# Performance work log

Hardware: AMD Instinct MI355X
Metric: run time of the kernel (lower is better)

The kernel has to match this reference:

```python
import jax, jax.numpy as jnp
import numpy as np

B, C, H, W = 4, 256, 128, 128
D = 256            # attention hidden_dim (== C, so no output_proj)
HID = 1024         # mlp hidden = int(C * 4.0)
EPS = 1e-5


def setup_inputs() -> dict:
    key = jax.random.key(0)
    ks = jax.random.split(key, 16)
    s = 0.02
    return {
        "x": jax.random.normal(ks[0], (B, C, H, W), jnp.float32),
        "wq": jax.random.normal(ks[1], (C, D), jnp.float32) * s,
        "bq": jnp.zeros((D,), jnp.float32),
        "wk": jax.random.normal(ks[2], (C, D), jnp.float32) * s,
        "bk": jnp.zeros((D,), jnp.float32),
        "wv": jax.random.normal(ks[3], (C, D), jnp.float32) * s,
        "bv": jnp.zeros((D,), jnp.float32),
        "ln1_g": jnp.ones((C,), jnp.float32),
        "ln1_b": jnp.zeros((C,), jnp.float32),
        "ln2_g": jnp.ones((C,), jnp.float32),
        "ln2_b": jnp.zeros((C,), jnp.float32),
        "fc1_w": jax.random.normal(ks[4], (C, HID), jnp.float32) * s,
        "fc1_b": jnp.zeros((HID,), jnp.float32),
        "fc2_w": jax.random.normal(ks[5], (HID, C), jnp.float32) * s,
        "fc2_b": jnp.zeros((C,), jnp.float32),
    }


def _layernorm(x, g, b):
    m = jnp.mean(x, axis=-1, keepdims=True)
    v = jnp.mean(jnp.square(x - m), axis=-1, keepdims=True)
    return (x - m) * jax.lax.rsqrt(v + EPS) * g + b


def _neighborhoods(t):
    # t: [B,H,W,D] -> [B,H,W,9,D] 3x3 neighborhoods, zero-padded at borders
    tp = jnp.pad(t, ((0, 0), (1, 1), (1, 1), (0, 0)))
    h, w = t.shape[1], t.shape[2]
    return jnp.stack(
        [tp[:, dy:dy + h, dx:dx + w, :] for dy in range(3) for dx in range(3)],
        axis=3,
    )


def _valid_mask(h, w):
    # [H,W,9] bool: which of the 9 neighbors are inside the grid
    ys = jnp.arange(h)[:, None] * jnp.ones((1, w), jnp.int32)
    xs = jnp.arange(w)[None, :] * jnp.ones((h, 1), jnp.int32)
    top, bot = ys > 0, ys < h - 1
    lef, rig = xs > 0, xs < w - 1
    ones = jnp.ones((h, w), bool)
    return jnp.stack(
        [top & lef, top, top & rig, lef, ones, rig, bot & lef, bot, bot & rig],
        axis=-1,
    )


def reference(x, wq, bq, wk, bk, wv, bv, ln1_g, ln1_b, ln2_g, ln2_b,
              fc1_w, fc1_b, fc2_w, fc2_b):
    b_, c_, h_, w_ = x.shape
    xc = jnp.transpose(x, (0, 2, 3, 1))                    # [B,H,W,C]
    n1 = _layernorm(xc, ln1_g, ln1_b)
    q = n1 @ wq + bq                                       # [B,H,W,D]
    k = n1 @ wk + bk
    v = n1 @ wv + bv
    kn = _neighborhoods(k)                                  # [B,H,W,9,D]
    vn = _neighborhoods(v)
    scores = jnp.einsum('bhwd,bhwnd->bhwn', q, kn) / jnp.sqrt(jnp.float32(q.shape[-1]))
    mask = _valid_mask(h_, w_)                               # [H,W,9]
    scores = jnp.where(mask, scores, jnp.float32(-1e9))
    weights = jax.nn.softmax(scores, axis=-1)
    attn = jnp.einsum('bhwn,bhwnd->bhwd', weights, vn)       # [B,H,W,D]
    x1 = xc + attn                                           # residual 1
    n2 = _layernorm(x1, ln2_g, ln2_b)
    mlp = jax.nn.gelu(n2 @ fc1_w + fc1_b, approximate=False) @ fc2_w + fc2_b
    out = x1 + mlp
    return jnp.transpose(out, (0, 3, 1, 2))                  # [B,C,H,W]
```

## Files before the change

### kernel.cpp

```cpp
#include <hip/hip_runtime.h>
#include <hip/hip_bf16.h>
#include <math.h>

#define NPIX  65536
#define CCH   256
#define HWSZ  16384
#define WIDTH 128
#define HID   1024

typedef unsigned short u16;
typedef __bf16 bf16x8 __attribute__((ext_vector_type(8)));
typedef float  floatx4 __attribute__((ext_vector_type(4)));

__device__ __forceinline__ float bf2f(u16 u) {
  union { unsigned int i; float f; } c; c.i = ((unsigned int)u) << 16; return c.f;
}
__device__ __forceinline__ float bflo(unsigned int u) {
  union { unsigned int i; float f; } c; c.i = u << 16; return c.f;
}
__device__ __forceinline__ float bfhi(unsigned int u) {
  union { unsigned int i; float f; } c; c.i = u & 0xffff0000u; return c.f;
}
__device__ __forceinline__ u16 f2bf(float f) {
  union { float f; unsigned int i; } c; c.f = f;
  unsigned int x = c.i;
  x += 0x7fffu + ((x >> 16) & 1u);
  return (u16)(x >> 16);
}

__device__ __forceinline__ void async16(const void* g, void* l) {
  __builtin_amdgcn_global_load_lds(
      (const __attribute__((address_space(1))) void*)g,
      (__attribute__((address_space(3))) void*)l, 16, 0, 0);
}

__global__ __launch_bounds__(256) void wtrans_kernel(
    const float* __restrict__ src, u16* __restrict__ dst, int R, int C) {
  __shared__ float tile[32][33];
  const int tx = threadIdx.x & 31, ty = threadIdx.x >> 5;
  const int r0 = blockIdx.y * 32, c0 = blockIdx.x * 32;
#pragma unroll
  for (int i = 0; i < 32; i += 8)
    tile[ty + i][tx] = src[(size_t)(r0 + ty + i) * C + c0 + tx];
  __syncthreads();
#pragma unroll
  for (int i = 0; i < 32; i += 8)
    dst[(size_t)(c0 + ty + i) * R + r0 + tx] = f2bf(tile[tx][ty + i]);
}

__global__ __launch_bounds__(256) void ln1_kernel(
    const float* __restrict__ x, const float* __restrict__ g,
    const float* __restrict__ bb, u16* __restrict__ n1) {
  __shared__ float sx[32][257];
  __shared__ float sred[16][32];
  __shared__ float sm[32], sr[32];
  const int tx = threadIdx.x;
  const int p0 = blockIdx.x * 32;
  {
    const int pix = tx & 31, cpart = tx >> 5;
    const int p = p0 + pix;
    const int b = p >> 14, hw = p & (HWSZ - 1);
    const float* xb = x + ((size_t)b * CCH) * HWSZ + hw;
    float s = 0.f, s2 = 0.f;
#pragma unroll 4
    for (int i = 0; i < 32; i++) {
      const int c = cpart * 32 + i;
      const float v = xb[(size_t)c * HWSZ];
      sx[pix][c] = v;
      s += v; s2 += v * v;
    }
    sred[cpart][pix] = s; sred[8 + cpart][pix] = s2;
  }
  __syncthreads();
  if (tx < 32) {
    float s = 0.f, s2 = 0.f;
#pragma unroll
    for (int j = 0; j < 8; j++) { s += sred[j][tx]; s2 += sred[8 + j][tx]; }
    const float m = s * (1.0f / 256.0f);
    const float var = s2 * (1.0f / 256.0f) - m * m;
    sm[tx] = m; sr[tx] = rsqrtf(var + 1e-5f);
  }
  __syncthreads();
  const float gc = g[tx], bc = bb[tx];
#pragma unroll 4
  for (int i = 0; i < 32; i++) {
    const float v = (sx[i][tx] - sm[i]) * sr[i] * gc + bc;
    n1[(size_t)(p0 + i) * CCH + tx] = f2bf(v);
  }
}

__global__ __launch_bounds__(256) void res_ln2_kernel(
    const float* __restrict__ x, const u16* __restrict__ attn,
    const float* __restrict__ g, const float* __restrict__ bb,
    float* __restrict__ x1, u16* __restrict__ n2) {
  __shared__ float sx[32][257];
  __shared__ float sred[16][32];
  __shared__ float sm[32], sr[32];
  const int tx = threadIdx.x;
  const int p0 = blockIdx.x * 32;
  {
    const int pix = tx & 31, cpart = tx >> 5;
    const int p = p0 + pix;
    const int b = p >> 14, hw = p & (HWSZ - 1);
    const float* xb = x + ((size_t)b * CCH) * HWSZ + hw;
#pragma unroll 4
    for (int i = 0; i < 32; i++) {
      const int c = cpart * 32 + i;
      sx[pix][c] = xb[(size_t)c * HWSZ];
    }
  }
  __syncthreads();
#pragma unroll 4
  for (int i = 0; i < 32; i++) {
    const float v = sx[i][tx] + bf2f(attn[(size_t)(p0 + i) * CCH + tx]);
    sx[i][tx] = v;
    x1[(size_t)(p0 + i) * CCH + tx] = v;
  }
  __syncthreads();
  {
    const int pix = tx & 31, cpart = tx >> 5;
    float s = 0.f, s2 = 0.f;
#pragma unroll 4
    for (int i = 0; i < 32; i++) {
      const float v = sx[pix][cpart * 32 + i];
      s += v; s2 += v * v;
    }
    sred[cpart][pix] = s; sred[8 + cpart][pix] = s2;
  }
  __syncthreads();
  if (tx < 32) {
    float s = 0.f, s2 = 0.f;
#pragma unroll
    for (int j = 0; j < 8; j++) { s += sred[j][tx]; s2 += sred[8 + j][tx]; }
    const float m = s * (1.0f / 256.0f);
    const float var = s2 * (1.0f / 256.0f) - m * m;
    sm[tx] = m; sr[tx] = rsqrtf(var + 1e-5f);
  }
  __syncthreads();
  const float gc = g[tx], bc = bb[tx];
#pragma unroll 4
  for (int i = 0; i < 32; i++) {
    const float v = (sx[i][tx] - sm[i]) * sr[i] * gc + bc;
    n2[(size_t)(p0 + i) * CCH + tx] = f2bf(v);
  }
}

__global__ __launch_bounds__(256) void attn_kernel(
    const u16* __restrict__ q, const u16* __restrict__ k,
    const u16* __restrict__ v, u16* __restrict__ attn) {
  const int tid = threadIdx.x;
  const int wave = tid >> 6, lane = tid & 63;
  const int p = blockIdx.x * 4 + wave;
  const int hw = p & (HWSZ - 1);
  const int hh = hw >> 7, ww = hw & (WIDTH - 1);
  const size_t co = (size_t)p * CCH + lane * 4;
  const uint2 qr = *(const uint2*)(q + co);
  const float qf0 = bflo(qr.x), qf1 = bfhi(qr.x);
  const float qf2 = bflo(qr.y), qf3 = bfhi(qr.y);
  float sc[9];
#pragma unroll
  for (int n = 0; n < 9; n++) {
    const int dy = n / 3 - 1, dx = n % 3 - 1;
    const int y = hh + dy, x2 = ww + dx;
    float s = -1e30f;
    if (y >= 0 && y < 128 && x2 >= 0 && x2 < 128) {
      const uint2 kr = *(const uint2*)(k + co + dy * (WIDTH * CCH) + dx * CCH);
      float d = qf0 * bflo(kr.x) + qf1 * bfhi(kr.x)
              + qf2 * bflo(kr.y) + qf3 * bfhi(kr.y);
#pragma unroll
      for (int o = 32; o >= 1; o >>= 1) d += __shfl_xor(d, o, 64);
      s = d * 0.0625f;
    }
    sc[n] = s;
  }
  float mx = sc[0];
#pragma unroll
  for (int n = 1; n < 9; n++) mx = fmaxf(mx, sc[n]);
  float wgt[9], wsum = 0.f;
#pragma unroll
  for (int n = 0; n < 9; n++) { wgt[n] = __expf(sc[n] - mx); wsum += wgt[n]; }
  const float inv = 1.0f / wsum;
  float a0 = 0.f, a1 = 0.f, a2 = 0.f, a3 = 0.f;
#pragma unroll
  for (int n = 0; n < 9; n++) {
    const int dy = n / 3 - 1, dx = n % 3 - 1;
    const int y = hh + dy, x2 = ww + dx;
    if (y >= 0 && y < 128 && x2 >= 0 && x2 < 128) {
      const uint2 vr = *(const uint2*)(v + co + dy * (WIDTH * CCH) + dx * CCH);
      const float wn = wgt[n] * inv;
      a0 += wn * bflo(vr.x); a1 += wn * bfhi(vr.x);
      a2 += wn * bflo(vr.y); a3 += wn * bfhi(vr.y);
    }
  }
  uint2 o;
  o.x = ((unsigned int)f2bf(a1) << 16) | (unsigned int)f2bf(a0);
  o.y = ((unsigned int)f2bf(a3) << 16) | (unsigned int)f2bf(a2);
  *(uint2*)(attn + co) = o;
}

template <int EPI>
__global__ __launch_bounds__(256, 2) void gemm_kernel(
    const u16* __restrict__ A, const u16* __restrict__ BT,
    const float* __restrict__ bias, const float* __restrict__ x1,
    u16* __restrict__ outb, float* __restrict__ outf, int K, int Nn) {
  __shared__ u16 sA[4096];
  __shared__ u16 sB[4096];
  const int tid = threadIdx.x;
  const int wave = tid >> 6;
  const int lane = tid & 63;
  const int quad = lane >> 4;
  const int l16 = lane & 15;
  const int m0 = blockIdx.x * 128;
  const int n0 = blockIdx.y * 128;
  const int wr = (wave >> 1) * 64;
  const int wc = (wave & 1) * 64;

  floatx4 acc[4][4];
#pragma unroll
  for (int i = 0; i < 4; i++)
#pragma unroll
    for (int j = 0; j < 4; j++) acc[i][j] = (floatx4){0.f, 0.f, 0.f, 0.f};

  const int ci0 = tid, ci1 = tid + 256;
  const u16* aP0 = A + (size_t)(m0 + (ci0 >> 2)) * K + (ci0 & 3) * 8;
  const u16* aP1 = A + (size_t)(m0 + (ci1 >> 2)) * K + (ci1 & 3) * 8;
  const u16* bP0 = BT + (size_t)(n0 + (ci0 >> 2)) * K + (ci0 & 3) * 8;
  const u16* bP1 = BT + (size_t)(n0 + (ci1 >> 2)) * K + (ci1 & 3) * 8;
  u16* sA0 = &sA[(wave * 64) * 8];
  u16* sA1 = &sA[(256 + wave * 64) * 8];
  u16* sB0 = &sB[(wave * 64) * 8];
  u16* sB1 = &sB[(256 + wave * 64) * 8];

  for (int k0 = 0; k0 < K; k0 += 32) {
    async16(aP0 + k0, sA0);
    async16(aP1 + k0, sA1);
    async16(bP0 + k0, sB0);
    async16(bP1 + k0, sB1);
    __syncthreads();
    bf16x8 af[4], bfv[4];
#pragma unroll
    for (int mi = 0; mi < 4; mi++)
      af[mi] = *(const bf16x8*)&sA[(wr + mi * 16 + l16) * 32 + quad * 8];
#pragma unroll
    for (int ni = 0; ni < 4; ni++)
      bfv[ni] = *(const bf16x8*)&sB[(wc + ni * 16 + l16) * 32 + quad * 8];
#pragma unroll
    for (int mi = 0; mi < 4; mi++)
#pragma unroll
      for (int ni = 0; ni < 4; ni++)
        acc[mi][ni] = __builtin_amdgcn_mfma_f32_16x16x32_bf16(
            af[mi], bfv[ni], acc[mi][ni], 0, 0, 0);
    __syncthreads();
  }

#pragma unroll
  for (int mi = 0; mi < 4; mi++) {
#pragma unroll
    for (int ni = 0; ni < 4; ni++) {
      const int col = n0 + wc + ni * 16 + l16;
      const float bs = bias[col];
#pragma unroll
      for (int r = 0; r < 4; r++) {
        const int row = m0 + wr + mi * 16 + quad * 4 + r;
        float val = acc[mi][ni][r] + bs;
        if (EPI == 0) {
          outb[(size_t)row * Nn + col] = f2bf(val);
        } else if (EPI == 1) {
          val = 0.5f * val * (1.0f + erff(val * 0.70710678118654752f));
          outb[(size_t)row * Nn + col] = f2bf(val);
        } else {
          val += x1[(size_t)row * CCH + col];
          const int b = row >> 14, hw = row & (HWSZ - 1);
          outf[((size_t)(b * CCH + col)) * HWSZ + hw] = val;
        }
      }
    }
  }
}

extern "C" void kernel_launch(void* const* d_in, const int* in_sizes, int n_in,
                              void* d_out, int out_size, void* d_ws, size_t ws_size,
                              hipStream_t stream) {
  const float* x    = (const float*)d_in[0];
  const float* wq   = (const float*)d_in[1];
  const float* bq   = (const float*)d_in[2];
  const float* wk   = (const float*)d_in[3];
  const float* bk   = (const float*)d_in[4];
  const float* wv   = (const float*)d_in[5];
  const float* bv   = (const float*)d_in[6];
  const float* ln1g = (const float*)d_in[7];
  const float* ln1b = (const float*)d_in[8];
  const float* ln2g = (const float*)d_in[9];
  const float* ln2b = (const float*)d_in[10];
  const float* fc1w = (const float*)d_in[11];
  const float* fc1b = (const float*)d_in[12];
  const float* fc2w = (const float*)d_in[13];
  const float* fc2b = (const float*)d_in[14];
  float* out = (float*)d_out;

  char* ws = (char*)d_ws;
  const size_t MB = (size_t)1 << 20;
  float* x1  = (float*)(ws);
  u16* hbuf  = (u16*)(ws + 64 * MB);
  u16* kbuf  = (u16*)(ws + 64 * MB);
  u16* vbuf  = (u16*)(ws + 96 * MB);
  u16* n1    = (u16*)(ws + 128 * MB);
  u16* attnb = n1;
  u16* qbuf  = (u16*)(ws + 192 * MB);
  u16* n2    = qbuf;
  u16* wqT   = (u16*)(ws + 224 * MB);
  u16* wkT   = wqT + 256 * 256;
  u16* wvT   = wkT + 256 * 256;
  u16* f1T   = wvT + 256 * 256;
  u16* f2T   = f1T + 1024 * 256;

  dim3 blk(256);
  wtrans_kernel<<<dim3(8, 8), blk, 0, stream>>>(wq, wqT, 256, 256);
  wtrans_kernel<<<dim3(8, 8), blk, 0, stream>>>(wk, wkT, 256, 256);
  wtrans_kernel<<<dim3(8, 8), blk, 0, stream>>>(wv, wvT, 256, 256);
  wtrans_kernel<<<dim3(32, 8), blk, 0, stream>>>(fc1w, f1T, 256, 1024);
  wtrans_kernel<<<dim3(8, 32), blk, 0, stream>>>(fc2w, f2T, 1024, 256);

  ln1_kernel<<<NPIX / 32, blk, 0, stream>>>(x, ln1g, ln1b, n1);

  gemm_kernel<0><<<dim3(512, 2), blk, 0, stream>>>(n1, wqT, bq, nullptr, qbuf, nullptr, 256, 256);
  gemm_kernel<0><<<dim3(512, 2), blk, 0, stream>>>(n1, wkT, bk, nullptr, kbuf, nullptr, 256, 256);
  gemm_kernel<0><<<dim3(512, 2), blk, 0, stream>>>(n1, wvT, bv, nullptr, vbuf, nullptr, 256, 256);

  attn_kernel<<<NPIX / 4, blk, 0, stream>>>(qbuf, kbuf, vbuf, attnb);

  res_ln2_kernel<<<NPIX / 32, blk, 0, stream>>>(x, attnb, ln2g, ln2b, x1, n2);

  gemm_kernel<1><<<dim3(512, 8), blk, 0, stream>>>(n2, f1T, fc1b, nullptr, hbuf, nullptr, 256, HID);
  gemm_kernel<2><<<dim3(512, 2), blk, 0, stream>>>(hbuf, f2T, fc2b, x1, nullptr, out, HID, 256);
}
```

Before: 489.4 us.

## Fuse QKV GEMMs, keep A tile in registers, use tanh GELU

Concatenates the Q/K/V weights and biases so a single GEMM writes an interleaved [pix,768] QKV buffer, and adapts the attention kernel to read from it. Replaces the old LDS-tiled GEMM with a new kernel that holds the 128-row A tile in registers and streams 64-column B chunks through padded LDS. One block covers all output columns, so A is read from global memory once. The fc1 epilogue swaps the exact erf GELU for the tanh approximation, which changes numerics relative to the reference (approximate=False). The register-resident A fragments may raise register pressure, and each B chunk has only one sync-separated stage with no double buffering.

```diff
diff --git a/kernel.cpp b/kernel.cpp
--- a/kernel.cpp
+++ b/kernel.cpp
@@ -46,6 +46,15 @@
 #pragma unroll
   for (int i = 0; i < 32; i += 8)
     dst[(size_t)(c0 + ty + i) * R + r0 + tx] = f2bf(tile[tx][ty + i]);
+}
+
+__global__ __launch_bounds__(256) void concat_bias_kernel(
+    const float* __restrict__ bq, const float* __restrict__ bk,
+    const float* __restrict__ bv, float* __restrict__ dst) {
+  const int i = blockIdx.x * 256 + threadIdx.x;
+  if (i < 256) dst[i] = bq[i];
+  else if (i < 512) dst[i] = bk[i - 256];
+  else if (i < 768) dst[i] = bv[i - 512];
 }
 
 __global__ __launch_bounds__(256) void ln1_kernel(
@@ -146,15 +155,14 @@
 }
 
 __global__ __launch_bounds__(256) void attn_kernel(
-    const u16* __restrict__ q, const u16* __restrict__ k,
-    const u16* __restrict__ v, u16* __restrict__ attn) {
+    const u16* __restrict__ qkv, u16* __restrict__ attn) {
   const int tid = threadIdx.x;
   const int wave = tid >> 6, lane = tid & 63;
   const int p = blockIdx.x * 4 + wave;
   const int hw = p & (HWSZ - 1);
   const int hh = hw >> 7, ww = hw & (WIDTH - 1);
-  const size_t co = (size_t)p * CCH + lane * 4;
-  const uint2 qr = *(const uint2*)(q + co);
+  const u16* rowp = qkv + (size_t)p * 768 + lane * 4;
+  const uint2 qr = *(const uint2*)rowp;
   const float qf0 = bflo(qr.x), qf1 = bfhi(qr.x);
   const float qf2 = bflo(qr.y), qf3 = bfhi(qr.y);
   float sc[9];
@@ -164,7 +172,7 @@
     const int y = hh + dy, x2 = ww + dx;
     float s = -1e30f;
     if (y >= 0 && y < 128 && x2 >= 0 && x2 < 128) {
-      const uint2 kr = *(const uint2*)(k + co + dy * (WIDTH * CCH) + dx * CCH);
+      const uint2 kr = *(const uint2*)(rowp + 256 + (dy * WIDTH + dx) * 768);
       float d = qf0 * bflo(kr.x) + qf1 * bfhi(kr.x)
               + qf2 * bflo(kr.y) + qf3 * bfhi(kr.y);
 #pragma unroll
@@ -186,7 +194,7 @@
     const int dy = n / 3 - 1, dx = n % 3 - 1;
     const int y = hh + dy, x2 = ww + dx;
     if (y >= 0 && y < 128 && x2 >= 0 && x2 < 128) {
-      const uint2 vr = *(const uint2*)(v + co + dy * (WIDTH * CCH) + dx * CCH);
+      const uint2 vr = *(const uint2*)(rowp + 512 + (dy * WIDTH + dx) * 768);
       const float wn = wgt[n] * inv;
       a0 += wn * bflo(vr.x); a1 += wn * bfhi(vr.x);
       a2 += wn * bflo(vr.y); a3 += wn * bfhi(vr.y);
@@ -195,86 +203,140 @@
   uint2 o;
   o.x = ((unsigned int)f2bf(a1) << 16) | (unsigned int)f2bf(a0);
   o.y = ((unsigned int)f2bf(a3) << 16) | (unsigned int)f2bf(a2);
-  *(uint2*)(attn + co) = o;
-}
-
-template <int EPI>
-__global__ __launch_bounds__(256, 2) void gemm_kernel(
+  *(uint2*)(attn + (size_t)p * CCH + lane * 4) = o;
+}
+
+template <int NCH, int KCH, int KT, int EPI>
+__global__ __launch_bounds__(256, 2) void gemm_regA(
     const u16* __restrict__ A, const u16* __restrict__ BT,
     const float* __restrict__ bias, const float* __restrict__ x1,
-    u16* __restrict__ outb, float* __restrict__ outf, int K, int Nn) {
-  __shared__ u16 sA[4096];
-  __shared__ u16 sB[4096];
-  const int tid = threadIdx.x;
-  const int wave = tid >> 6;
-  const int lane = tid & 63;
-  const int quad = lane >> 4;
-  const int l16 = lane & 15;
+    u16* __restrict__ outb, float* __restrict__ outf, int Kglb) {
+  constexpr int KS   = KT / 32;
+  constexpr int K16  = KT / 8;
+  constexpr int CPC  = 512 / KT;
+  constexpr int CSU  = KT;
+  constexpr int GSU  = (8 * KT * 2 + 64) / 2;
+  constexpr int NACC = (KCH > 1) ? NCH : 1;
+  __shared__ u16 sB[8 * GSU];
+
+  const int tid  = threadIdx.x;
+  const int wave = tid >> 6, lane = tid & 63;
+  const int quad = lane >> 4, l16 = lane & 15;
   const int m0 = blockIdx.x * 128;
-  const int n0 = blockIdx.y * 128;
-  const int wr = (wave >> 1) * 64;
-  const int wc = (wave & 1) * 64;
-
-  floatx4 acc[4][4];
-#pragma unroll
-  for (int i = 0; i < 4; i++)
-#pragma unroll
-    for (int j = 0; j < 4; j++) acc[i][j] = (floatx4){0.f, 0.f, 0.f, 0.f};
-
-  const int ci0 = tid, ci1 = tid + 256;
-  const u16* aP0 = A + (size_t)(m0 + (ci0 >> 2)) * K + (ci0 & 3) * 8;
-  const u16* aP1 = A + (size_t)(m0 + (ci1 >> 2)) * K + (ci1 & 3) * 8;
-  const u16* bP0 = BT + (size_t)(n0 + (ci0 >> 2)) * K + (ci0 & 3) * 8;
-  const u16* bP1 = BT + (size_t)(n0 + (ci1 >> 2)) * K + (ci1 & 3) * 8;
-  u16* sA0 = &sA[(wave * 64) * 8];
-  u16* sA1 = &sA[(256 + wave * 64) * 8];
-  u16* sB0 = &sB[(wave * 64) * 8];
-  u16* sB1 = &sB[(256 + wave * 64) * 8];
-
-  for (int k0 = 0; k0 < K; k0 += 32) {
-    async16(aP0 + k0, sA0);
-    async16(aP1 + k0, sA1);
-    async16(bP0 + k0, sB0);
-    async16(bP1 + k0, sB1);
-    __syncthreads();
-    bf16x8 af[4], bfv[4];
+  const int wr  = (wave & 1) * 64;
+  const int wcq = (wave >> 1) * 32;
+
+  const int c0 = wcq + l16, c1 = c0 + 16;
+  const int sb0 = (c0 >> 3) * GSU + (c0 & 7) * CSU;
+  const int sb1 = (c1 >> 3) * GSU + (c1 & 7) * CSU;
+
+  const int stc   = wave * 16;
+  const int stcol = (lane * 16) / (KT * 2);
+  const int stk   = lane & (K16 - 1);
+
+  const u16* aRow = A + (size_t)(m0 + wr + l16) * Kglb + quad * 8;
+
+  bf16x8 afr[4][KS];
+  floatx4 acc[NACC][4][2];
+
+  auto stage = [&](int idx) {
+    const int kc = idx / NCH, ch = idx % NCH;
+    const u16* gB = BT + kc * KT + stk * 8;
+#pragma unroll
+    for (int i = 0; i < 16 / CPC; i++) {
+      const int cc = stc + i * CPC;
+      async16(gB + (size_t)(ch * 64 + cc + stcol) * Kglb,
+              sB + (cc >> 3) * GSU + (cc & 7) * CSU);
+    }
+  };
+  auto loadA = [&](int kc) {
 #pragma unroll
     for (int mi = 0; mi < 4; mi++)
-      af[mi] = *(const bf16x8*)&sA[(wr + mi * 16 + l16) * 32 + quad * 8];
-#pragma unroll
-    for (int ni = 0; ni < 4; ni++)
-      bfv[ni] = *(const bf16x8*)&sB[(wc + ni * 16 + l16) * 32 + quad * 8];
+#pragma unroll
+      for (int ks = 0; ks < KS; ks++)
+        afr[mi][ks] = *(const bf16x8*)(aRow + (size_t)mi * 16 * Kglb + kc * KT + ks * 32);
+  };
+  auto compute = [&](int ci) {
+#pragma unroll
+    for (int ks = 0; ks < KS; ks++) {
+      const int ko = (ks * 4 + quad) * 8;
+      const bf16x8 b0 = *(const bf16x8*)&sB[sb0 + ko];
+      const bf16x8 b1 = *(const bf16x8*)&sB[sb1 + ko];
+#pragma unroll
+      for (int mi = 0; mi < 4; mi++) {
+        acc[ci][mi][0] = __builtin_amdgcn_mfma_f32_16x16x32_bf16(
+            afr[mi][ks], b0, acc[ci][mi][0], 0, 0, 0);
+        acc[ci][mi][1] = __builtin_amdgcn_mfma_f32_16x16x32_bf16(
+            afr[mi][ks], b1, acc[ci][mi][1], 0, 0, 0);
+      }
+    }
+  };
+  auto epilogue = [&](int ci, int ch) {
 #pragma unroll
     for (int mi = 0; mi < 4; mi++)
 #pragma unroll
-      for (int ni = 0; ni < 4; ni++)
-        acc[mi][ni] = __builtin_amdgcn_mfma_f32_16x16x32_bf16(
-            af[mi], bfv[ni], acc[mi][ni], 0, 0, 0);
-    __syncthreads();
-  }
-
-#pragma unroll
-  for (int mi = 0; mi < 4; mi++) {
-#pragma unroll
-    for (int ni = 0; ni < 4; ni++) {
-      const int col = n0 + wc + ni * 16 + l16;
-      const float bs = bias[col];
-#pragma unroll
-      for (int r = 0; r < 4; r++) {
-        const int row = m0 + wr + mi * 16 + quad * 4 + r;
-        float val = acc[mi][ni][r] + bs;
-        if (EPI == 0) {
-          outb[(size_t)row * Nn + col] = f2bf(val);
-        } else if (EPI == 1) {
-          val = 0.5f * val * (1.0f + erff(val * 0.70710678118654752f));
-          outb[(size_t)row * Nn + col] = f2bf(val);
-        } else {
-          val += x1[(size_t)row * CCH + col];
-          const int b = row >> 14, hw = row & (HWSZ - 1);
-          outf[((size_t)(b * CCH + col)) * HWSZ + hw] = val;
+      for (int ni = 0; ni < 2; ni++) {
+        const int col = ch * 64 + wcq + ni * 16 + l16;
+        const float bs = bias[col];
+#pragma unroll
+        for (int r = 0; r < 4; r++) {
+          const int row = m0 + wr + mi * 16 + quad * 4 + r;
+          float val = acc[ci][mi][ni][r] + bs;
+          if constexpr (EPI == 0) {
+            outb[(size_t)row * 768 + col] = f2bf(val);
+          } else if constexpr (EPI == 1) {
+            const float t = 0.7978845608028654f * (val + 0.044715f * val * val * val);
+            const float e = __expf(2.0f * t);
+            const float th = 1.0f - 2.0f / (e + 1.0f);
+            val = 0.5f * val * (1.0f + th);
+            outb[(size_t)row * HID + col] = f2bf(val);
+          } else {
+            val += x1[(size_t)row * CCH + col];
+            outf[((size_t)((row >> 14) * CCH + col)) * HWSZ + (row & (HWSZ - 1))] = val;
+          }
         }
       }
-    }
+  };
+
+  if constexpr (KCH == 1) {
+    stage(0);
+    loadA(0);
+#pragma unroll 1
+    for (int ch = 0; ch < NCH; ++ch) {
+      __syncthreads();
+#pragma unroll
+      for (int mi = 0; mi < 4; mi++)
+#pragma unroll
+        for (int ni = 0; ni < 2; ni++)
+          acc[0][mi][ni] = (floatx4){0.f, 0.f, 0.f, 0.f};
+      compute(0);
+      __syncthreads();
+      if (ch + 1 < NCH) stage(ch + 1);
+      epilogue(0, ch);
+    }
+  } else {
+    stage(0);
+#pragma unroll
+    for (int ci = 0; ci < NACC; ci++)
+#pragma unroll
+      for (int mi = 0; mi < 4; mi++)
+#pragma unroll
+        for (int ni = 0; ni < 2; ni++)
+          acc[ci][mi][ni] = (floatx4){0.f, 0.f, 0.f, 0.f};
+#pragma unroll 1
+    for (int kc = 0; kc < KCH; ++kc) {
+      loadA(kc);
+#pragma unroll
+      for (int ch = 0; ch < NCH; ++ch) {
+        __syncthreads();
+        compute(ch);
+        __syncthreads();
+        const int nxt = kc * NCH + ch + 1;
+        if (nxt < KCH * NCH) stage(nxt);
+      }
+    }
+#pragma unroll
+    for (int ch = 0; ch < NCH; ++ch) epilogue(ch, ch);
   }
 }
 
@@ -300,37 +362,37 @@
 
   char* ws = (char*)d_ws;
   const size_t MB = (size_t)1 << 20;
-  float* x1  = (float*)(ws);
-  u16* hbuf  = (u16*)(ws + 64 * MB);
-  u16* kbuf  = (u16*)(ws + 64 * MB);
-  u16* vbuf  = (u16*)(ws + 96 * MB);
-  u16* n1    = (u16*)(ws + 128 * MB);
-  u16* attnb = n1;
-  u16* qbuf  = (u16*)(ws + 192 * MB);
-  u16* n2    = qbuf;
-  u16* wqT   = (u16*)(ws + 224 * MB);
-  u16* wkT   = wqT + 256 * 256;
-  u16* wvT   = wkT + 256 * 256;
-  u16* f1T   = wvT + 256 * 256;
-  u16* f2T   = f1T + 1024 * 256;
+  float* x1   = (float*)(ws);
+  u16* qkv    = (u16*)(ws + 64 * MB);
+  u16* hbuf   = (u16*)(ws + 64 * MB);
+  u16* n1     = (u16*)(ws + 160 * MB);
+  u16* attnb  = n1;
+  u16* n2     = (u16*)(ws + 192 * MB);
+  u16* wqkvT  = (u16*)(ws + 224 * MB);
+  u16* f1T    = wqkvT + 768 * 256;
+  u16* f2T    = f1T + 1024 * 256;
+  float* bqkv = (float*)(f2T + 256 * 1024);
 
   dim3 blk(256);
-  wtrans_kernel<<<dim3(8, 8), blk, 0, stream>>>(wq, wqT, 256, 256);
-  wtrans_kernel<<<dim3(8, 8), blk, 0, stream>>>(wk, wkT, 256, 256);
-  wtrans_kernel<<<dim3(8, 8), blk, 0, stream>>>(wv, wvT, 256, 256);
+  wtrans_kernel<<<dim3(8, 8), blk, 0, stream>>>(wq, wqkvT, 256, 256);
+  wtrans_kernel<<<dim3(8, 8), blk, 0, stream>>>(wk, wqkvT + 256 * 256, 256, 256);
+  wtrans_kernel<<<dim3(8, 8), blk, 0, stream>>>(wv, wqkvT + 512 * 256, 256, 256);
   wtrans_kernel<<<dim3(32, 8), blk, 0, stream>>>(fc1w, f1T, 256, 1024);
   wtrans_kernel<<<dim3(8, 32), blk, 0, stream>>>(fc2w, f2T, 1024, 256);
+  concat_bias_kernel<<<dim3(3), blk, 0, stream>>>(bq, bk, bv, bqkv);
 
   ln1_kernel<<<NPIX / 32, blk, 0, stream>>>(x, ln1g, ln1b, n1);
 
-  gemm_kernel<0><<<dim3(512, 2), blk, 0, stream>>>(n1, wqT, bq, nullptr, qbuf, nullptr, 256, 256);
-  gemm_kernel<0><<<dim3(512, 2), blk, 0, stream>>>(n1, wkT, bk, nullptr, kbuf, nullptr, 256, 256);
-  gemm_kernel<0><<<dim3(512, 2), blk, 0, stream>>>(n1, wvT, bv, nullptr, vbuf, nullptr, 256, 256);
-
-  attn_kernel<<<NPIX / 4, blk, 0, stream>>>(qbuf, kbuf, vbuf, attnb);
+  gemm_regA<12, 1, 256, 0><<<dim3(512), blk, 0, stream>>>(
+      n1, wqkvT, bqkv, nullptr, qkv, nullptr, 256);
+
+  attn_kernel<<<NPIX / 4, blk, 0, stream>>>(qkv, attnb);
 
   res_ln2_kernel<<<NPIX / 32, blk, 0, stream>>>(x, attnb, ln2g, ln2b, x1, n2);
 
-  gemm_kernel<1><<<dim3(512, 8), blk, 0, stream>>>(n2, f1T, fc1b, nullptr, hbuf, nullptr, 256, HID);
-  gemm_kernel<2><<<dim3(512, 2), blk, 0, stream>>>(hbuf, f2T, fc2b, x1, nullptr, out, HID, 256);
-}
+  gemm_regA<16, 1, 256, 1><<<dim3(512), blk, 0, stream>>>(
+      n2, f1T, fc1b, nullptr, hbuf, nullptr, 256);
+
+  gemm_regA<4, 8, 128, 2><<<dim3(512), blk, 0, stream>>>(
+      hbuf, f2T, fc2b, x1, nullptr, out, 1024);
+}
```

New measurement: 485.8 us. No clear change (-0.7%).
